# Performance work log

Hardware: AMD Instinct MI355X
Metric: run time of the kernel (lower is better)

The kernel has to match this reference:

```python
import jax, jax.numpy as jnp
import numpy as np

B, T, F, H, TL = 256, 512, 64, 1024, 64

def _gru_step(h, x, W_ih, W_hh, b_ih, b_hh):
    # torch nn.GRU cell semantics
    gi = x @ W_ih.T + b_ih          # [B, 3H]
    gh = h @ W_hh.T + b_hh          # [B, 3H]
    ir, iz, inn = jnp.split(gi, 3, axis=-1)
    hr, hz, hn = jnp.split(gh, 3, axis=-1)
    r = jax.nn.sigmoid(ir + hr)
    z = jax.nn.sigmoid(iz + hz)
    n = jnp.tanh(inn + r * hn)
    return (1.0 - z) * n + z * h

def setup_inputs() -> dict:
    key = jax.random.key(0)
    ks = jax.random.split(key, 12)
    s_e = 1.0 / np.sqrt(H)
    u = lambda k, shp: jax.random.uniform(k, shp, jnp.float32, -s_e, s_e)
    return {
        "x": jax.random.normal(ks[0], (B, T, F), jnp.float32),
        "enc_W_ih": u(ks[1], (3 * H, F)),
        "enc_W_hh": u(ks[2], (3 * H, H)),
        "enc_b_ih": u(ks[3], (3 * H,)),
        "enc_b_hh": u(ks[4], (3 * H,)),
        "dec_W_ih": u(ks[5], (3 * H, 1)),
        "dec_W_hh": u(ks[6], (3 * H, H)),
        "dec_b_ih": u(ks[7], (3 * H,)),
        "dec_b_hh": u(ks[8], (3 * H,)),
        "fc_W": u(ks[9], (1, H)),
        "fc_b": u(ks[10], (1,)),
    }

def reference(x, enc_W_ih, enc_W_hh, enc_b_ih, enc_b_hh,
              dec_W_ih, dec_W_hh, dec_b_ih, dec_b_hh, fc_W, fc_b):
    b = x.shape[0]
    h0 = jnp.zeros((b, H), x.dtype)

    # encoder: sequential GRU over time
    def enc_step(h, xt):
        return _gru_step(h, xt, enc_W_ih, enc_W_hh, enc_b_ih, enc_b_hh), None
    h_enc, _ = jax.lax.scan(enc_step, h0, jnp.swapaxes(x, 0, 1))  # [B, H]

    inp0 = jnp.zeros((b, 1), x.dtype)
    def dec_step(carry, _):
        h, inp = carry
        h = _gru_step(h, inp, dec_W_ih, dec_W_hh, dec_b_ih, dec_b_hh)
        out = h @ fc_W.T + fc_b  # [B, 1]
        return (h, out), out
    _, outs = jax.lax.scan(dec_step, (h_enc, inp0), None, length=TL)  # [TL, B, 1]
    return jnp.swapaxes(outs, 0, 1)  # [B, TL, 1]
```

## Files before the change

kernel.cpp:

```cpp
#include <hip/hip_runtime.h>

#define B_  256
#define T_  512
#define F_  64
#define H_  1024
#define TL_ 64

typedef _Float16 half8 __attribute__((ext_vector_type(8)));
typedef float   floatx4 __attribute__((ext_vector_type(4)));
typedef unsigned long long ull;

#define MFMA(a, b, c) __builtin_amdgcn_mfma_f32_16x16x32_f16(a, b, c, 0, 0, 0)

#define WF_E   0UL
#define WF_D   6291456UL
#define WF_I   12582912UL
#define HP     12976128UL
#define PSTR   524288UL
#define PB     15073280UL
#define BARS   15204352UL

__device__ __forceinline__ void sta8(void* p, ull v) {
  __hip_atomic_store((ull*)p, v, __ATOMIC_RELAXED, __HIP_MEMORY_SCOPE_AGENT);
}
__device__ __forceinline__ void sta4(unsigned* p, unsigned v) {
  __hip_atomic_store(p, v, __ATOMIC_RELAXED, __HIP_MEMORY_SCOPE_AGENT);
}
__device__ __forceinline__ float lda4f(const float* p) {
  return __hip_atomic_load(p, __ATOMIC_RELAXED, __HIP_MEMORY_SCOPE_AGENT);
}
__device__ __forceinline__ unsigned lda4u(const unsigned* p) {
  return __hip_atomic_load(p, __ATOMIC_RELAXED, __HIP_MEMORY_SCOPE_AGENT);
}

__global__ void gru_setup(const float* __restrict__ WhhE,
                          const float* __restrict__ WhhD,
                          const float* __restrict__ WihE,
                          char* __restrict__ ws) {
  int t = blockIdx.x * 256 + threadIdx.x;
  if (t < 512) ((unsigned int*)(ws + BARS))[t] = 0u;
  const int NW = 3 * 64 * 32 * 4 * 16;
  if (t < 2 * NW) {
    const float* W = (t < NW) ? WhhE : WhhD;
    size_t dst = (t < NW) ? WF_E : WF_D;
    int c = (t < NW) ? t : t - NW;
    int r = c & 15, q = (c >> 4) & 3, kb = (c >> 6) & 31, gj = c >> 11;
    int row = (gj >> 6) * H_ + (gj & 63) * 16 + r;
    const float* src = W + (size_t)row * H_ + kb * 32 + q * 8;
    half8 v;
#pragma unroll
    for (int i = 0; i < 8; ++i) v[i] = (_Float16)src[i];
    *(half8*)(ws + dst + (size_t)c * 16) = v;
  } else if (t < 2 * NW + 3 * 64 * 2 * 4 * 16) {
    int c = t - 2 * NW;
    int r = c & 15, q = (c >> 4) & 3, kc = (c >> 6) & 1, gj = c >> 7;
    int row = (gj >> 6) * H_ + (gj & 63) * 16 + r;
    const float* src = WihE + (size_t)row * F_ + kc * 32 + q * 8;
    half8 v;
#pragma unroll
    for (int i = 0; i < 8; ++i) v[i] = (_Float16)src[i];
    *(half8*)(ws + WF_I + (size_t)c * 16) = v;
  }
}

__device__ __forceinline__ void gbar(unsigned int* cnt, unsigned int target) {
  __syncthreads();
  if (threadIdx.x == 0) {
    __hip_atomic_fetch_add(cnt, 1u, __ATOMIC_RELAXED,
                           __HIP_MEMORY_SCOPE_AGENT);
    while (__hip_atomic_load(cnt, __ATOMIC_RELAXED,
                             __HIP_MEMORY_SCOPE_AGENT) < target)
      __builtin_amdgcn_s_sleep(1);
  }
  __syncthreads();
}

__global__ __launch_bounds__(512, 2) void gru_main(
    const float* __restrict__ x,
    const float* __restrict__ bih_e, const float* __restrict__ bhh_e,
    const float* __restrict__ Wih_d,
    const float* __restrict__ bih_d, const float* __restrict__ bhh_d,
    const float* __restrict__ fcW, const float* __restrict__ fcb,
    float* __restrict__ out, char* __restrict__ ws) {

  __shared__ __align__(128) char atile[32768];
  __shared__ float red[4 * 64 * 17];
  __shared__ __align__(16) char otile[2048];
  __shared__ float inp_lds[16];

  const int tid = threadIdx.x;
  const int L = tid & 63;
  const int w = tid >> 6;
  const int jp = w & 3;
  const int kh = w >> 2;
  const int bx = blockIdx.x;
  const int rg = bx & 15;
  const int cb = bx >> 4;
  const int r = L & 15;
  const int q = L >> 4;
  const int jg = cb * 4 + jp;
  const int jc = jg * 16 + r;

  unsigned int* line = (unsigned int*)(ws + BARS) + (size_t)rg * 32;
  unsigned int* tgs = line + 8;

  const size_t slab = (size_t)rg * 32768;

  if (tid < 256) {
    sta8(ws + HP + slab + (size_t)cb * 2048 + (size_t)tid * 8, 0ull);
  }

  float hold[4] = {0.f, 0.f, 0.f, 0.f};
  const float fcb_s = *fcb;
  const float fcw_l = fcW[jc];

  gbar(line, 16);

  for (int phase = 0; phase < 2; ++phase) {
    half8 bW[48];
    {
      const char* wf = ws + (phase ? WF_D : WF_E);
#pragma unroll
      for (int g = 0; g < 3; ++g)
#pragma unroll
        for (int kk = 0; kk < 16; ++kk)
          bW[g * 16 + kk] = *(const half8*)(
              wf + (size_t)((g * 64 + jg) * 32 + kh * 16 + kk) * 1024 +
              (size_t)L * 16);
#pragma unroll
      for (int i = 0; i < 48; ++i) asm volatile("" : "+v"(bW[i]));
    }
    const float* bih = phase ? bih_d : bih_e;
    const float* bhh = phase ? bhh_d : bhh_e;
    const float b_r  = bih[jc]          + bhh[jc];
    const float b_z  = bih[H_ + jc]     + bhh[H_ + jc];
    const float b_in = bih[2 * H_ + jc];
    const float b_hn = bhh[2 * H_ + jc];
    float wd_r = 0.f, wd_z = 0.f, wd_n = 0.f;
    if (phase) {
      wd_r = Wih_d[jc]; wd_z = Wih_d[H_ + jc]; wd_n = Wih_d[2 * H_ + jc];
    }

    const char* wfi = ws + WF_I + (size_t)L * 16;

    const int nsteps = phase ? TL_ : T_;
    for (int d = 0; d < nsteps; ++d) {
      const int s = phase ? T_ + d : d;
      const unsigned tnext = (unsigned)(s + 1);

      {
        const char* srcbase = ws + HP + (size_t)(s & 1) * PSTR + slab;
#pragma unroll
        for (int c = 0; c < 4; ++c) {
          const int seg = w * 4 + c;
          const char* src = srcbase + (size_t)seg * 1024 + (size_t)L * 16;
          __builtin_amdgcn_global_load_lds(
              (const __attribute__((address_space(1))) void*)src,
              (__attribute__((address_space(3))) void*)(atile + seg * 1024),
              16, 0, 17);
        }
      }

      floatx4 a0 = {0.f, 0.f, 0.f, 0.f}, a1 = {0.f, 0.f, 0.f, 0.f};
      floatx4 aI = {0.f, 0.f, 0.f, 0.f};
      if (!phase && kh == 1) {
        const float* xp = x + ((size_t)(rg * 16 + r) * T_ + s) * F_ + q * 8;
#pragma unroll
        for (int kc = 0; kc < 2; ++kc) {
          floatx4 x0 = *(const floatx4*)(xp + kc * 32);
          floatx4 x1 = *(const floatx4*)(xp + kc * 32 + 4);
          half8 xa;
#pragma unroll
          for (int i = 0; i < 4; ++i) {
            xa[i] = (_Float16)x0[i];
            xa[4 + i] = (_Float16)x1[i];
          }
          a0 = MFMA(xa, *(const half8*)(wfi +
                   (size_t)((0 * 64 + jg) * 2 + kc) * 1024), a0);
          a1 = MFMA(xa, *(const half8*)(wfi +
                   (size_t)((1 * 64 + jg) * 2 + kc) * 1024), a1);
          aI = MFMA(xa, *(const half8*)(wfi +
                   (size_t)((2 * 64 + jg) * 2 + kc) * 1024), aI);
        }
      }
      if (phase && tid < 16) {
        float sum = 0.f;
        if (d > 0) {
          const float* pb =
              (const float*)(ws + PB) + (size_t)((d + 1) & 1) * 64 * 256;
          int row = rg * 16 + tid;
          float a = fcb_s;
          for (int jj = 0; jj < 64; ++jj) a += lda4f(&pb[jj * 256 + row]);
          sum = a;
          if (cb == 0) out[(size_t)row * TL_ + (d - 1)] = a;
        }
        inp_lds[tid] = sum;
      }
      __syncthreads();

      floatx4 a2 = {0.f, 0.f, 0.f, 0.f};

#pragma unroll
      for (int kk = 0; kk < 16; ++kk) {
        const int kb = kh * 16 + kk;
        half8 ahi = *(const half8*)(atile + kb * 1024 + L * 16);
        a0 = MFMA(ahi, bW[kk], a0);
        a1 = MFMA(ahi, bW[16 + kk], a1);
        a2 = MFMA(ahi, bW[32 + kk], a2);
      }

      if (kh == 1) {
        float* rd = &red[(jp * 64 + L) * 17];
#pragma unroll
        for (int i = 0; i < 4; ++i) {
          rd[i] = a0[i];
          rd[4 + i] = a1[i];
          rd[8 + i] = a2[i];
        }
        if (!phase) {
#pragma unroll
          for (int i = 0; i < 4; ++i) rd[12 + i] = aI[i];
        }
      }
      __syncthreads();

      if (kh == 0) {
        const float* rd = &red[(jp * 64 + L) * 17];
        const size_t tbase = (size_t)(jp >> 1) * 1024 +
                             (size_t)((jp & 1) * 2 + (r >> 3)) * 256 +
                             (size_t)(r & 7) * 2;
        float pv[4];
#pragma unroll
        for (int i = 0; i < 4; ++i) {
          float rpre = a0[i] + rd[i] + b_r;
          float zpre = a1[i] + rd[4 + i] + b_z;
          float hn   = a2[i] + rd[8 + i] + b_hn;
          float inn  = b_in + (phase ? 0.f : rd[12 + i]);
          if (phase) {
            float inp = inp_lds[q * 4 + i];
            rpre += inp * wd_r;
            zpre += inp * wd_z;
            inn  += inp * wd_n;
          }
          float rg_ = 1.f / (1.f + __expf(-rpre));
          float zg = 1.f / (1.f + __expf(-zpre));
          float t2 = __expf(-2.f * (inn + rg_ * hn));
          float ng = 2.f / (1.f + t2) - 1.f;
          float hnew = (1.f - zg) * ng + zg * hold[i];
          hold[i] = hnew;
          *(_Float16*)(otile + tbase + (size_t)(q * 4 + i) * 16) =
              (_Float16)hnew;
          pv[i] = hnew * fcw_l;
        }
        if (phase) {
#pragma unroll
          for (int i = 0; i < 4; ++i) {
            float v = pv[i];
            v += __shfl_xor(v, 1);
            v += __shfl_xor(v, 2);
            v += __shfl_xor(v, 4);
            v += __shfl_xor(v, 8);
            if (r == 0) {
              float* pb = (float*)(ws + PB) + (size_t)(d & 1) * 64 * 256;
              __hip_atomic_store(&pb[jg * 256 + (rg * 16 + q * 4 + i)], v,
                                 __ATOMIC_RELAXED, __HIP_MEMORY_SCOPE_AGENT);
            }
          }
        }
        ull v8 = *(const ull*)(otile + (size_t)jp * 512 + (size_t)L * 8);
        sta8(ws + HP + (size_t)((s + 1) & 1) * PSTR + slab +
                 (size_t)cb * 2048 + (size_t)jp * 512 + (size_t)L * 8,
             v8);
      }

      __syncthreads();
      if (tid == 0) sta4(tgs + cb, tnext);
      if (w == 0) {
        for (;;) {
          unsigned tag = (L < 16) ? lda4u(tgs + L) : tnext;
          if (__all((int)(tag >= tnext))) break;
          __builtin_amdgcn_s_sleep(1);
        }
      }
      __syncthreads();
    }
  }

  if (cb == 0 && tid < 16) {
    const float* pb =
        (const float*)(ws + PB) + (size_t)((TL_ - 1) & 1) * 64 * 256;
    int row = rg * 16 + tid;
    float a = fcb_s;
    for (int jj = 0; jj < 64; ++jj) a += lda4f(&pb[jj * 256 + row]);
    out[(size_t)row * TL_ + (TL_ - 1)] = a;
  }
}

extern "C" void kernel_launch(void* const* d_in, const int* in_sizes, int n_in,
                              void* d_out, int out_size, void* d_ws,
                              size_t ws_size, hipStream_t stream) {
  const float* x     = (const float*)d_in[0];
  const float* WihE  = (const float*)d_in[1];
  const float* WhhE  = (const float*)d_in[2];
  const float* bihE  = (const float*)d_in[3];
  const float* bhhE  = (const float*)d_in[4];
  const float* WihD  = (const float*)d_in[5];
  const float* WhhD  = (const float*)d_in[6];
  const float* bihD  = (const float*)d_in[7];
  const float* bhhD  = (const float*)d_in[8];
  const float* fcW   = (const float*)d_in[9];
  const float* fcb   = (const float*)d_in[10];
  float* outp = (float*)d_out;
  char* ws = (char*)d_ws;

  gru_setup<<<3168, 256, 0, stream>>>(WhhE, WhhD, WihE, ws);

  gru_main<<<dim3(256), dim3(512), 0, stream>>>(
      x, bihE, bhhE, WihD, bihD, bhhD, fcW, fcb, outp, ws);
}
```

Baseline: 2.607 ms.

## Replace per-step all-block barrier with per-producer readiness polling and incremental loads

Drops the end-of-step wait for all 16 column blocks to publish their tags. Wave 0 now polls the tags at the start of the next step and issues global-to-LDS loads for each producer's hidden-state slice as soon as that producer is ready, which overlaps the loads with waiting on slower blocks. The decoder input reduction moves into wave 0, and the other waves do the input MFMAs meanwhile. This trims one __syncthreads per step and loosens the lockstep coupling. In exchange, correctness now depends on the tag ordering and memory visibility of the double-buffered hidden state, with possible write-after-read hazards now that blocks can run ahead.

Result: slower. 3.351 ms (+28.5%).

```diff
diff --git a/kernel.cpp b/kernel.cpp
--- a/kernel.cpp
+++ b/kernel.cpp
@@ -146,19 +146,48 @@
     const int nsteps = phase ? TL_ : T_;
     for (int d = 0; d < nsteps; ++d) {
       const int s = phase ? T_ + d : d;
-      const unsigned tnext = (unsigned)(s + 1);
-
-      {
+
+      if (w == 0) {
         const char* srcbase = ws + HP + (size_t)(s & 1) * PSTR + slab;
-#pragma unroll
-        for (int c = 0; c < 4; ++c) {
-          const int seg = w * 4 + c;
-          const char* src = srcbase + (size_t)seg * 1024 + (size_t)L * 16;
-          __builtin_amdgcn_global_load_lds(
-              (const __attribute__((address_space(1))) void*)src,
-              (__attribute__((address_space(3))) void*)(atile + seg * 1024),
-              16, 0, 17);
-        }
+        const unsigned gate = (unsigned)s;
+        unsigned done = 0;
+        for (;;) {
+          unsigned tag = (L < 16) ? lda4u(tgs + L) : 0xFFFFFFFFu;
+          ull rdy = __ballot((int)(tag >= gate));
+          unsigned newr = ((unsigned)rdy & 0xFFFFu) & ~done;
+          while (newr) {
+            const int j = __builtin_ctz(newr);
+            newr &= newr - 1;
+#pragma unroll
+            for (int t2 = 0; t2 < 2; ++t2) {
+              const int seg = j * 2 + t2;
+              const char* src =
+                  srcbase + (size_t)seg * 1024 + (size_t)L * 16;
+              __builtin_amdgcn_global_load_lds(
+                  (const __attribute__((address_space(1))) void*)src,
+                  (__attribute__((address_space(3))) void*)(atile +
+                                                           seg * 1024),
+                  16, 0, 17);
+            }
+            done |= 1u << j;
+          }
+          if (done == 0xFFFFu) break;
+          __builtin_amdgcn_s_sleep(1);
+        }
+        if (phase && L < 16) {
+          float sum = 0.f;
+          if (d > 0) {
+            const float* pb =
+                (const float*)(ws + PB) + (size_t)((d + 1) & 1) * 64 * 256;
+            int row = rg * 16 + L;
+            float a = fcb_s;
+            for (int jj = 0; jj < 64; ++jj) a += lda4f(&pb[jj * 256 + row]);
+            sum = a;
+            if (cb == 0) out[(size_t)row * TL_ + (d - 1)] = a;
+          }
+          inp_lds[L] = sum;
+        }
+        asm volatile("s_waitcnt vmcnt(0)" ::: "memory");
       }
 
       floatx4 a0 = {0.f, 0.f, 0.f, 0.f}, a1 = {0.f, 0.f, 0.f, 0.f};
@@ -182,19 +211,6 @@
           aI = MFMA(xa, *(const half8*)(wfi +
                    (size_t)((2 * 64 + jg) * 2 + kc) * 1024), aI);
         }
-      }
-      if (phase && tid < 16) {
-        float sum = 0.f;
-        if (d > 0) {
-          const float* pb =
-              (const float*)(ws + PB) + (size_t)((d + 1) & 1) * 64 * 256;
-          int row = rg * 16 + tid;
-          float a = fcb_s;
-          for (int jj = 0; jj < 64; ++jj) a += lda4f(&pb[jj * 256 + row]);
-          sum = a;
-          if (cb == 0) out[(size_t)row * TL_ + (d - 1)] = a;
-        }
-        inp_lds[tid] = sum;
       }
       __syncthreads();
 
@@ -274,19 +290,13 @@
       }
 
       __syncthreads();
-      if (tid == 0) sta4(tgs + cb, tnext);
-      if (w == 0) {
-        for (;;) {
-          unsigned tag = (L < 16) ? lda4u(tgs + L) : tnext;
-          if (__all((int)(tag >= tnext))) break;
-          __builtin_amdgcn_s_sleep(1);
-        }
-      }
-      __syncthreads();
+      if (tid == 0) sta4(tgs + cb, (unsigned)(s + 1));
     }
   }
 
   if (cb == 0 && tid < 16) {
+    while (lda4u(tgs + tid) < (unsigned)(T_ + TL_))
+      __builtin_amdgcn_s_sleep(1);
     const float* pb =
         (const float*)(ws + PB) + (size_t)((TL_ - 1) & 1) * 64 * 256;
     int row = rg * 16 + tid;
```
